# Optimization experiments

Measured on AMD Instinct MI355X. Metric: run time of the kernel, lower is better.

## Reference

```python
import jax, jax.numpy as jnp
import numpy as np

IN_FEATURES = 4096
OUT_FEATURES = 4096


def setup_inputs() -> dict:
    key = jax.random.key(0)
    k_x, k_w, k_b = jax.random.split(key, 3)
    inp = {
        "input": jax.random.normal(k_x, (4, 2048, IN_FEATURES), dtype=jnp.float32),
        # learned int8 weight table [out_features, in_features]
        "weight_int8": jax.random.randint(k_w, (OUT_FEATURES, IN_FEATURES), -128, 128, dtype=jnp.int32).astype(jnp.int8),
        # per-tensor dequant scales (scalars, as in the module buffers)
        "scale": jnp.asarray(0.01, dtype=jnp.float32),
        "x_scale": jnp.asarray(0.05, dtype=jnp.float32),
        "bias": jax.random.normal(k_b, (OUT_FEATURES,), dtype=jnp.float32) * 0.02,
    }
    return inp


def reference(input, weight_int8, scale, x_scale, bias):
    # --- quantize activations per-tensor to int8 (W8A8 path) ---
    x_int8 = jnp.clip(jnp.round(input / x_scale), -128, 127).astype(jnp.int8)
    in_shape = input.shape
    x_flat = x_int8.reshape(-1, in_shape[-1])  # [B*S, in]
    # contract x_flat[k] with weight_int8[n, k] -> [B*S, out]
    out_i32 = jax.lax.dot_general(
        x_flat, weight_int8,
        dimension_numbers=(((1,), (1,)), ((), ())),
        preferred_element_type=jnp.int32,
    )
    # --- dequant epilogue: combined scale, reshape, bias ---
    out = out_i32.astype(input.dtype) * (scale * x_scale)
    out = out.reshape(*in_shape[:-1], weight_int8.shape[0])
    out = out + bias
    return out
```

## Files before the change

### kernel.cpp

```cpp
#include <hip/hip_runtime.h>

#define KDIM 4096
#define NDIM 4096
#define BM 256
#define BN 256
#define BK 128
#define NTILE (KDIM / BK)

using i32x4 = __attribute__((ext_vector_type(4))) int;

__device__ __forceinline__ void g2l16(const void* g, void* l) {
  __builtin_amdgcn_global_load_lds(
      (const __attribute__((address_space(1))) void*)g,
      (__attribute__((address_space(3))) void*)l,
      16, 0, 0);
}

__global__ void w8l_detect(const int* __restrict__ w32, int* __restrict__ flag) {
  __shared__ int s;
  const int t = threadIdx.x;
  if (t == 0) s = 1;
  __syncthreads();
  bool oob = false;
#pragma unroll
  for (int i = 0; i < 16; ++i) {
    int v = w32[t * 16 + i];
    if (v < -128 || v > 127) oob = true;
  }
  if (oob) atomicAnd(&s, 0);
  __syncthreads();
  if (t == 0) *flag = s;
}

__global__ void w8l_pack(const void* __restrict__ wsrc, const int* __restrict__ flag,
                         signed char* __restrict__ wq) {
  if (*flag == 0) return;
  const int t = blockIdx.x * blockDim.x + threadIdx.x;
  const int4* s = (const int4*)wsrc;
  int4 a = s[t * 4 + 0], b = s[t * 4 + 1], c = s[t * 4 + 2], d = s[t * 4 + 3];
  int4 o;
  o.x = (a.x & 255) | ((a.y & 255) << 8) | ((a.z & 255) << 16) | ((a.w & 255) << 24);
  o.y = (b.x & 255) | ((b.y & 255) << 8) | ((b.z & 255) << 16) | ((b.w & 255) << 24);
  o.z = (c.x & 255) | ((c.y & 255) << 8) | ((c.z & 255) << 16) | ((c.w & 255) << 24);
  o.w = (d.x & 255) | ((d.y & 255) << 8) | ((d.z & 255) << 16) | ((d.w & 255) << 24);
  ((int4*)wq)[t] = o;
}

__global__ void w8l_quant(const float* __restrict__ x, const float* __restrict__ xs,
                          signed char* __restrict__ xq) {
  const int t = blockIdx.x * blockDim.x + threadIdx.x;
  const float s = *xs;
  const float4* x4 = (const float4*)x;
  int4 o;
  int* op = (int*)&o;
#pragma unroll
  for (int q = 0; q < 4; ++q) {
    float4 f = x4[t * 4 + q];
    int v0 = __float2int_rn(f.x / s);
    int v1 = __float2int_rn(f.y / s);
    int v2 = __float2int_rn(f.z / s);
    int v3 = __float2int_rn(f.w / s);
    v0 = v0 < -128 ? -128 : (v0 > 127 ? 127 : v0);
    v1 = v1 < -128 ? -128 : (v1 > 127 ? 127 : v1);
    v2 = v2 < -128 ? -128 : (v2 > 127 ? 127 : v2);
    v3 = v3 < -128 ? -128 : (v3 > 127 ? 127 : v3);
    op[q] = (v0 & 255) | ((v1 & 255) << 8) | ((v2 & 255) << 16) | ((v3 & 255) << 24);
  }
  ((int4*)xq)[t] = o;
}

__global__ __launch_bounds__(512, 2) void w8l_gemmp(
    const signed char* __restrict__ Aq,
    const signed char* __restrict__ Wraw, const signed char* __restrict__ Wpk,
    const int* __restrict__ flag,
    const float* __restrict__ scale, const float* __restrict__ xscale,
    const float* __restrict__ bias, float* __restrict__ out, int nbn) {
  __shared__ signed char lds[131072];

  const signed char* __restrict__ Wq = (*flag) ? Wpk : Wraw;

  const int tid = threadIdx.x;
  const int lane = tid & 63;
  const int wid = tid >> 6;
  const int wr = wid >> 2;
  const int wc = wid & 3;
  const int l15 = lane & 15;
  const int l4 = lane >> 4;

  const int nwg = gridDim.x;
  const int cpx = nwg >> 3;
  const int bid = blockIdx.x;
  const int swz = (bid & 7) * cpx + (bid >> 3);
  const int bm = swz / nbn, bn = swz % nbn;
  const int m0 = bm * BM, n0 = bn * BN;

  const unsigned lin = (unsigned)tid * 16u;
  const unsigned r_in = lin >> 7;
  const unsigned c16 = (lin >> 4) & 7;
  const unsigned swcol = ((c16 ^ (r_in & 7)) << 4);
  const signed char* agp = Aq + (size_t)(m0 + r_in) * KDIM + swcol;
  const signed char* wgp = Wq + (size_t)(n0 + r_in) * KDIM + swcol;
  const unsigned ldsoff_thr = r_in * 128u + c16 * 16u;

#define ISSUE_TILE(t)                                                       \
  do {                                                                      \
    const int t_ = (t);                                                     \
    const size_t koff_ = (size_t)t_ * BK;                                   \
    signed char* lb_ = lds + (unsigned)(t_ & 1) * 65536u + ldsoff_thr;      \
    _Pragma("unroll") for (int u = 0; u < 4; ++u)                           \
      g2l16(agp + (size_t)(u * 64) * KDIM + koff_, lb_ + u * 8192);         \
    _Pragma("unroll") for (int u = 0; u < 4; ++u)                           \
      g2l16(wgp + (size_t)(u * 64) * KDIM + koff_, lb_ + 32768 + u * 8192); \
  } while (0)

#define LDFRAG(base, row, sl) \
  (*(const i32x4*)((base) + (row) * 128 + (((((sl) * 4) + l4) ^ ((row) & 7)) * 16)))

#define READ_A(dst, base, sl)                                          \
  _Pragma("unroll") for (int i = 0; i < 8; ++i)                        \
      dst[i] = LDFRAG((base), wr * 128 + i * 16 + l15, (sl));
#define READ_B(dst, base, sl)                                          \
  _Pragma("unroll") for (int j = 0; j < 4; ++j)                        \
      dst[j] = LDFRAG((base), wc * 64 + j * 16 + l15, (sl));
#define MFMA_CLUSTER(av, bv)                                           \
  __builtin_amdgcn_s_setprio(1);                                       \
  _Pragma("unroll") for (int i = 0; i < 8; ++i)                        \
      _Pragma("unroll") for (int j = 0; j < 4; ++j)                    \
          acc[i][j] = __builtin_amdgcn_mfma_i32_16x16x64_i8(           \
              av[i], bv[j], acc[i][j], 0, 0, 0);                       \
  __builtin_amdgcn_s_setprio(0);

  i32x4 acc[8][4] = {};
  i32x4 aE[8], bE[4], aO[8], bO[4];

  ISSUE_TILE(0);
  ISSUE_TILE(1);
  asm volatile("s_waitcnt vmcnt(8)" ::: "memory");
  __builtin_amdgcn_s_barrier();
  __builtin_amdgcn_sched_barrier(0);
  READ_A(aE, lds, 0);
  READ_B(bE, lds + 32768, 0);
  __builtin_amdgcn_sched_barrier(0);

#pragma unroll 1
  for (int kt = 0; kt < NTILE; ++kt) {
    const signed char* Ab = &lds[(kt & 1) * 65536];
    const signed char* Bb = Ab + 32768;

    READ_A(aO, Ab, 1);
    READ_B(bO, Bb, 1);
    __builtin_amdgcn_sched_barrier(0);
    MFMA_CLUSTER(aE, bE);
    __builtin_amdgcn_sched_barrier(0);
    asm volatile("s_waitcnt lgkmcnt(0)" ::: "memory");
    __builtin_amdgcn_sched_barrier(0);

    if (kt + 1 < NTILE) {
      asm volatile("s_waitcnt vmcnt(0)" ::: "memory");
      __builtin_amdgcn_s_barrier();
      __builtin_amdgcn_sched_barrier(0);
      const signed char* An = &lds[((kt + 1) & 1) * 65536];
      const signed char* Bn = An + 32768;
      READ_A(aE, An, 0);
      READ_B(bE, Bn, 0);
      if (kt + 2 < NTILE) ISSUE_TILE(kt + 2);
      __builtin_amdgcn_sched_barrier(0);
    }
    MFMA_CLUSTER(aO, bO);
    __builtin_amdgcn_sched_barrier(0);
  }

  const float cs = scale[0] * xscale[0];
#pragma unroll
  for (int j = 0; j < 4; ++j) {
    const int n = n0 + wc * 64 + j * 16 + l15;
    const float bj = bias[n];
#pragma unroll
    for (int i = 0; i < 8; ++i) {
      const int m = m0 + wr * 128 + i * 16 + l4 * 4;
      float* o = out + (size_t)m * NDIM + n;
#pragma unroll
      for (int v = 0; v < 4; ++v)
        o[(size_t)v * NDIM] = (float)acc[i][j][v] * cs + bj;
    }
  }
#undef ISSUE_TILE
#undef LDFRAG
#undef READ_A
#undef READ_B
#undef MFMA_CLUSTER
}

extern "C" void kernel_launch(void* const* d_in, const int* in_sizes, int n_in,
                              void* d_out, int out_size, void* d_ws, size_t ws_size,
                              hipStream_t stream) {
  const float* x = (const float*)d_in[0];
  const void* w = d_in[1];
  const float* scale = (const float*)d_in[2];
  const float* xscale = (const float*)d_in[3];
  const float* bias = (const float*)d_in[4];
  float* out = (float*)d_out;

  const int M = in_sizes[0] / KDIM;

  int* flag = (int*)d_ws;
  signed char* wq = (signed char*)d_ws + 256;
  signed char* aq = wq + (size_t)NDIM * KDIM;

  const size_t need = 256 + (size_t)NDIM * KDIM + (size_t)M * KDIM;
  if (ws_size < need) return;

  w8l_detect<<<1, 256, 0, stream>>>((const int*)w, flag);
  w8l_pack<<<(NDIM * KDIM / 16) / 256, 256, 0, stream>>>(w, flag, wq);
  w8l_quant<<<(M * KDIM / 16) / 256, 256, 0, stream>>>(x, xscale, aq);

  const int nbn = NDIM / BN;
  w8l_gemmp<<<(M / BM) * nbn, 512, 0, stream>>>(
      aq, (const signed char*)w, wq, flag, scale, xscale, bias, out, nbn);
}
```

Measured before the change: 181.5 us.

## Restructure int8 GEMM to 128x256 tiles with triple-buffered LDS pipeline

Reworks the int8 GEMM kernel from 256x256x128 tiles with 8 waves and double buffering to 128x256x64 tiles with 4 waves and three LDS buffers. Each wave now computes a 64x128 sub-tile, and global-to-LDS loads for tile k+2 are issued right after a single barrier per iteration. The LDS swizzle and fragment addressing are redone for the 64-byte rows. The aim is a smaller LDS footprint, better occupancy and more grid blocks, at the cost of a shorter K step that gives less compute per barrier and less reuse per tile.

```diff
diff --git a/kernel.cpp b/kernel.cpp
--- a/kernel.cpp
+++ b/kernel.cpp
@@ -2,10 +2,12 @@
 
 #define KDIM 4096
 #define NDIM 4096
-#define BM 256
+#define BM 128
 #define BN 256
-#define BK 128
+#define BK 64
 #define NTILE (KDIM / BK)
+#define BUFSZ 24576
+#define NBUF 3
 
 using i32x4 = __attribute__((ext_vector_type(4))) int;
 
@@ -69,23 +71,23 @@
   ((int4*)xq)[t] = o;
 }
 
-__global__ __launch_bounds__(512, 2) void w8l_gemmp(
+__global__ __launch_bounds__(256, 2) void w8l_gemm(
     const signed char* __restrict__ Aq,
     const signed char* __restrict__ Wraw, const signed char* __restrict__ Wpk,
     const int* __restrict__ flag,
     const float* __restrict__ scale, const float* __restrict__ xscale,
     const float* __restrict__ bias, float* __restrict__ out, int nbn) {
-  __shared__ signed char lds[131072];
+  __shared__ signed char lds[NBUF * BUFSZ];
 
   const signed char* __restrict__ Wq = (*flag) ? Wpk : Wraw;
 
   const int tid = threadIdx.x;
   const int lane = tid & 63;
   const int wid = tid >> 6;
-  const int wr = wid >> 2;
-  const int wc = wid & 3;
+  const int wr = wid >> 1;
+  const int wc = wid & 1;
   const int l15 = lane & 15;
-  const int l4 = lane >> 4;
+  const int l4 = (lane >> 4) & 3;
 
   const int nwg = gridDim.x;
   const int cpx = nwg >> 3;
@@ -94,101 +96,86 @@
   const int bm = swz / nbn, bn = swz % nbn;
   const int m0 = bm * BM, n0 = bn * BN;
 
-  const unsigned lin = (unsigned)tid * 16u;
-  const unsigned r_in = lin >> 7;
-  const unsigned c16 = (lin >> 4) & 7;
-  const unsigned swcol = ((c16 ^ (r_in & 7)) << 4);
+  const unsigned r_in = (unsigned)tid >> 2;
+  const unsigned c16 = (unsigned)tid & 3;
+  const unsigned s_in = (r_in >> 1) & 3u;
+  const unsigned swcol = ((c16 ^ s_in) << 4);
   const signed char* agp = Aq + (size_t)(m0 + r_in) * KDIM + swcol;
   const signed char* wgp = Wq + (size_t)(n0 + r_in) * KDIM + swcol;
-  const unsigned ldsoff_thr = r_in * 128u + c16 * 16u;
-
-#define ISSUE_TILE(t)                                                       \
-  do {                                                                      \
-    const int t_ = (t);                                                     \
-    const size_t koff_ = (size_t)t_ * BK;                                   \
-    signed char* lb_ = lds + (unsigned)(t_ & 1) * 65536u + ldsoff_thr;      \
-    _Pragma("unroll") for (int u = 0; u < 4; ++u)                           \
-      g2l16(agp + (size_t)(u * 64) * KDIM + koff_, lb_ + u * 8192);         \
-    _Pragma("unroll") for (int u = 0; u < 4; ++u)                           \
-      g2l16(wgp + (size_t)(u * 64) * KDIM + koff_, lb_ + 32768 + u * 8192); \
+  const unsigned ldsoff = (unsigned)tid * 16u;
+
+#define ISSUE_TILE(t, buf)                                                   \
+  do {                                                                       \
+    const size_t koff_ = (size_t)(t) * BK;                                   \
+    signed char* lb_ = lds + (unsigned)(buf) * BUFSZ + ldsoff;               \
+    _Pragma("unroll") for (int u = 0; u < 2; ++u)                            \
+      g2l16(agp + (size_t)(u * 64) * KDIM + koff_, lb_ + u * 4096);          \
+    _Pragma("unroll") for (int u = 0; u < 4; ++u)                            \
+      g2l16(wgp + (size_t)(u * 64) * KDIM + koff_, lb_ + 8192 + u * 4096);   \
   } while (0)
 
-#define LDFRAG(base, row, sl) \
-  (*(const i32x4*)((base) + (row) * 128 + (((((sl) * 4) + l4) ^ ((row) & 7)) * 16)))
-
-#define READ_A(dst, base, sl)                                          \
-  _Pragma("unroll") for (int i = 0; i < 8; ++i)                        \
-      dst[i] = LDFRAG((base), wr * 128 + i * 16 + l15, (sl));
-#define READ_B(dst, base, sl)                                          \
-  _Pragma("unroll") for (int j = 0; j < 4; ++j)                        \
-      dst[j] = LDFRAG((base), wc * 64 + j * 16 + l15, (sl));
-#define MFMA_CLUSTER(av, bv)                                           \
-  __builtin_amdgcn_s_setprio(1);                                       \
-  _Pragma("unroll") for (int i = 0; i < 8; ++i)                        \
-      _Pragma("unroll") for (int j = 0; j < 4; ++j)                    \
-          acc[i][j] = __builtin_amdgcn_mfma_i32_16x16x64_i8(           \
-              av[i], bv[j], acc[i][j], 0, 0, 0);                       \
-  __builtin_amdgcn_s_setprio(0);
-
-  i32x4 acc[8][4] = {};
-  i32x4 aE[8], bE[4], aO[8], bO[4];
-
-  ISSUE_TILE(0);
-  ISSUE_TILE(1);
-  asm volatile("s_waitcnt vmcnt(8)" ::: "memory");
-  __builtin_amdgcn_s_barrier();
-  __builtin_amdgcn_sched_barrier(0);
-  READ_A(aE, lds, 0);
-  READ_B(bE, lds + 32768, 0);
-  __builtin_amdgcn_sched_barrier(0);
-
+  const unsigned slotoff = (unsigned)((l4 ^ ((l15 >> 1) & 3)) << 4);
+  const unsigned arow = (unsigned)((wr * 64 + l15) * 64) + slotoff;
+  const unsigned brow = (unsigned)((wc * 128 + l15) * 64) + slotoff + 8192u;
+
+  i32x4 acc[4][8] = {};
+  i32x4 af[4], bf[8];
+
+  ISSUE_TILE(0, 0);
+  ISSUE_TILE(1, 1);
+
+  int bufr = 0, bufi = 2;
 #pragma unroll 1
   for (int kt = 0; kt < NTILE; ++kt) {
-    const signed char* Ab = &lds[(kt & 1) * 65536];
-    const signed char* Bb = Ab + 32768;
-
-    READ_A(aO, Ab, 1);
-    READ_B(bO, Bb, 1);
-    __builtin_amdgcn_sched_barrier(0);
-    MFMA_CLUSTER(aE, bE);
+    if (kt + 2 < NTILE) {
+      asm volatile("s_waitcnt vmcnt(6)" ::: "memory");
+    } else {
+      asm volatile("s_waitcnt vmcnt(0)" ::: "memory");
+    }
+    __builtin_amdgcn_s_barrier();
+    __builtin_amdgcn_sched_barrier(0);
+
+    if (kt + 2 < NTILE) ISSUE_TILE(kt + 2, bufi);
+
+    const signed char* base = lds + (unsigned)bufr * BUFSZ;
+#pragma unroll
+    for (int mi = 0; mi < 4; ++mi)
+      af[mi] = *(const i32x4*)(base + arow + mi * 1024);
+#pragma unroll
+    for (int nj = 0; nj < 8; ++nj)
+      bf[nj] = *(const i32x4*)(base + brow + nj * 1024);
     __builtin_amdgcn_sched_barrier(0);
     asm volatile("s_waitcnt lgkmcnt(0)" ::: "memory");
     __builtin_amdgcn_sched_barrier(0);
 
-    if (kt + 1 < NTILE) {
-      asm volatile("s_waitcnt vmcnt(0)" ::: "memory");
-      __builtin_amdgcn_s_barrier();
-      __builtin_amdgcn_sched_barrier(0);
-      const signed char* An = &lds[((kt + 1) & 1) * 65536];
-      const signed char* Bn = An + 32768;
-      READ_A(aE, An, 0);
-      READ_B(bE, Bn, 0);
-      if (kt + 2 < NTILE) ISSUE_TILE(kt + 2);
-      __builtin_amdgcn_sched_barrier(0);
+    __builtin_amdgcn_s_setprio(1);
+#pragma unroll
+    for (int mi = 0; mi < 4; ++mi)
+#pragma unroll
+      for (int nj = 0; nj < 8; ++nj)
+        acc[mi][nj] = __builtin_amdgcn_mfma_i32_16x16x64_i8(af[mi], bf[nj], acc[mi][nj], 0, 0, 0);
+    __builtin_amdgcn_s_setprio(0);
+    __builtin_amdgcn_sched_barrier(0);
+
+    bufr = (bufr == 2) ? 0 : bufr + 1;
+    bufi = (bufi == 2) ? 0 : bufi + 1;
+  }
+
+  const float cs = scale[0] * xscale[0];
+#pragma unroll
+  for (int nj = 0; nj < 8; ++nj) {
+    const int n = n0 + wc * 128 + nj * 16 + l15;
+    const float bj = bias[n];
+#pragma unroll
+    for (int mi = 0; mi < 4; ++mi) {
+      const int m = m0 + wr * 64 + mi * 16 + l4 * 4;
+      float* o = out + (size_t)m * NDIM + n;
+#pragma unroll
+      for (int v = 0; v < 4; ++v)
+        o[(size_t)v * NDIM] = (float)acc[mi][nj][v] * cs + bj;
     }
-    MFMA_CLUSTER(aO, bO);
-    __builtin_amdgcn_sched_barrier(0);
-  }
-
-  const float cs = scale[0] * xscale[0];
-#pragma unroll
-  for (int j = 0; j < 4; ++j) {
-    const int n = n0 + wc * 64 + j * 16 + l15;
-    const float bj = bias[n];
-#pragma unroll
-    for (int i = 0; i < 8; ++i) {
-      const int m = m0 + wr * 128 + i * 16 + l4 * 4;
-      float* o = out + (size_t)m * NDIM + n;
-#pragma unroll
-      for (int v = 0; v < 4; ++v)
-        o[(size_t)v * NDIM] = (float)acc[i][j][v] * cs + bj;
-    }
   }
 #undef ISSUE_TILE
-#undef LDFRAG
-#undef READ_A
-#undef READ_B
-#undef MFMA_CLUSTER
 }
 
 extern "C" void kernel_launch(void* const* d_in, const int* in_sizes, int n_in,
@@ -215,6 +202,6 @@
   w8l_quant<<<(M * KDIM / 16) / 256, 256, 0, stream>>>(x, xscale, aq);
 
   const int nbn = NDIM / BN;
-  w8l_gemmp<<<(M / BM) * nbn, 512, 0, stream>>>(
+  w8l_gemm<<<(M / BM) * nbn, 256, 0, stream>>>(
       aq, (const signed char*)w, wq, flag, scale, xscale, bias, out, nbn);
 }
```

New measurement: 198.2 us. +9.2%, slower.
